# Performance work log

Measured on AMD Instinct MI355X. Metric: run time of the kernel, lower is better.

Reference implementation:

```python
import jax, jax.numpy as jnp
import numpy as np

EPS = 1e-05


def layer_norm(x, a, b):
    m = jnp.mean(x, axis=-1, keepdims=True)
    v = jnp.var(x, axis=-1, keepdims=True)
    return a * (x - m) / jnp.sqrt(v + EPS) + b


def setup_inputs() -> dict:
    key = jax.random.key(0)
    ks = jax.random.split(key, 16)
    b, n, d, h = 1, 384, 128, 128
    s = 1.0 / np.sqrt(d)
    inp = {
        "x": jax.random.normal(ks[0], (b, n, n, d), dtype=jnp.float32),
        "norm_a": jnp.ones((d,), jnp.float32),
        "norm_b": jnp.zeros((d,), jnp.float32),
        "Wl": jax.random.normal(ks[1], (d, h), jnp.float32) * s,
        "bl": jnp.zeros((h,), jnp.float32),
        "Wr": jax.random.normal(ks[2], (d, h), jnp.float32) * s,
        "br": jnp.zeros((h,), jnp.float32),
        "Wlg": jax.random.normal(ks[3], (d, h), jnp.float32) * s,
        "blg": jnp.ones((h,), jnp.float32),
        "Wrg": jax.random.normal(ks[4], (d, h), jnp.float32) * s,
        "brg": jnp.ones((h,), jnp.float32),
        "Wog": jax.random.normal(ks[5], (d, h), jnp.float32) * s,
        "bog": jnp.ones((h,), jnp.float32),
        "on_a": jnp.ones((h,), jnp.float32),
        "on_b": jnp.zeros((h,), jnp.float32),
        "Wo": jax.random.normal(ks[6], (h, d), jnp.float32) * s,
        "bo": jnp.zeros((d,), jnp.float32),
    }
    return inp


def reference(x, norm_a, norm_b, Wl, bl, Wr, br, Wlg, blg, Wrg, brg, Wog, bog, on_a, on_b, Wo, bo):
    n = x.shape[1]
    xn = layer_norm(x, norm_a, norm_b)
    left = (xn @ Wl + bl) * jax.nn.sigmoid(xn @ Wlg + blg)
    right = (xn @ Wr + br) * jax.nn.sigmoid(xn @ Wrg + brg)
    out_gate = jax.nn.sigmoid(xn @ Wog + bog)
    # ingoing mix: out[b,i,j,d] = sum_k left[b,k,j,d] * right[b,k,i,d], in fp32
    out = jnp.einsum('bkjd,bkid->bijd', left.astype(jnp.float32), right.astype(jnp.float32)) / n
    out = out.astype(x.dtype)
    out = layer_norm(out, on_a, on_b) * out_gate
    return out @ Wo + bo
```

## Files before the change

kernel.cpp:

```cpp
#include <hip/hip_runtime.h>
#include <hip/hip_bf16.h>

#define NN 384
#define DD 128
#define MM (NN*NN)
#define IDJ 49152

typedef __attribute__((ext_vector_type(8))) short short8;
typedef __attribute__((ext_vector_type(4))) float f32x4;

__device__ __forceinline__ unsigned short f2bf(float f){
  unsigned u = __float_as_uint(f);
  u += 0x7fffu + ((u >> 16) & 1u);
  return (unsigned short)(u >> 16);
}
__device__ __forceinline__ float bf2f(unsigned short u){
  return __uint_as_float(((unsigned)u) << 16);
}
__device__ __forceinline__ float sigm(float x){
  return 1.0f / (1.0f + __expf(-x));
}
__device__ __forceinline__ unsigned cvtpk(float lo, float hi){
  unsigned r;
  asm("v_cvt_pk_bf16_f32 %0, %1, %2" : "=v"(r) : "v"(lo), "v"(hi));
  return r;
}
__device__ __forceinline__ f32x4 mfma16(short8 a, short8 b, f32x4 c){
  return __builtin_amdgcn_mfma_f32_16x16x32_bf16(a, b, c, 0, 0, 0);
}
__device__ __forceinline__ void gll16(const void* g, void* l){
  __builtin_amdgcn_global_load_lds(
      (const __attribute__((address_space(1))) unsigned int*)g,
      (__attribute__((address_space(3))) unsigned int*)l, 16, 0, 0);
}

__global__ void k_prep(const float* __restrict__ Wl, const float* __restrict__ Wlg,
                       const float* __restrict__ Wr, const float* __restrict__ Wrg,
                       const float* __restrict__ Wog, const float* __restrict__ Wo,
                       unsigned short* __restrict__ Wcat, unsigned short* __restrict__ Wot){
  int n = blockIdx.x;
  if(n < 640){
    const float* src; int col;
    if(n < 128){ src = Wl;  col = n; }
    else if(n < 256){ src = Wlg; col = n-128; }
    else if(n < 384){ src = Wr;  col = n-256; }
    else if(n < 512){ src = Wrg; col = n-384; }
    else            { src = Wog; col = n-512; }
    for(int k = threadIdx.x; k < 128; k += 64)
      Wcat[n*128 + k] = f2bf(src[k*128 + col]);
  } else {
    int c = n - 640;
    for(int k = threadIdx.x; k < 128; k += 64)
      Wot[c*128 + k] = f2bf(Wo[k*128 + c]);
  }
}

__global__ __launch_bounds__(256, 3) void k_lng(
    const float* __restrict__ x, const float* __restrict__ na,
    const float* __restrict__ nb, const unsigned short* __restrict__ Wcat,
    const float* __restrict__ bog,
    unsigned short* __restrict__ xn, unsigned short* __restrict__ gate){
  __shared__ char lds[32768];
  const int tid = threadIdx.x;
  const int wid = tid >> 6, lane = tid & 63;
  const int lrow = lane & 15, lgrp = lane >> 4;
  const long m0 = (long)blockIdx.x * 128;

  float2 a2 = *(const float2*)(na + lane*2);
  float2 b2 = *(const float2*)(nb + lane*2);

  #pragma unroll 2
  for(int b4 = 0; b4 < 8; ++b4){
    float2 v[4];
    #pragma unroll
    for(int s = 0; s < 4; ++s)
      v[s] = *(const float2*)(x + (m0 + wid*32 + b4*4 + s)*DD + lane*2);
    #pragma unroll
    for(int s = 0; s < 4; ++s){
      int r = wid*32 + b4*4 + s;
      float sm = v[s].x + v[s].y, sq = v[s].x*v[s].x + v[s].y*v[s].y;
      #pragma unroll
      for(int m = 32; m >= 1; m >>= 1){ sm += __shfl_xor(sm,m); sq += __shfl_xor(sq,m); }
      float mean = sm*(1.f/128.f);
      float var  = sq*(1.f/128.f) - mean*mean;
      float rstd = rsqrtf(var + 1e-5f);
      unsigned pk = cvtpk(a2.x*(v[s].x-mean)*rstd + b2.x,
                          a2.y*(v[s].y-mean)*rstd + b2.y);
      *(unsigned*)(xn + (m0+r)*DD + lane*2) = pk;
      *(unsigned*)(&lds[r*256 + ((lane*4) ^ ((r&7)<<4))]) = pk;
    }
  }
  __syncthreads();

  f32x4 acc[2][8];
  #pragma unroll
  for(int cf = 0; cf < 2; ++cf){
    int c0 = wid*32 + cf*16 + lgrp*4;
    float4 b4v = *(const float4*)(bog + c0);
    #pragma unroll
    for(int mf = 0; mf < 8; ++mf) acc[cf][mf] = (f32x4){b4v.x,b4v.y,b4v.z,b4v.w};
  }
  #pragma unroll
  for(int ks = 0; ks < 4; ++ks){
    short8 af0 = *(const short8*)(Wcat + (512 + wid*32 + lrow)*DD + ks*32 + lgrp*8);
    short8 af1 = *(const short8*)(Wcat + (512 + wid*32 + 16 + lrow)*DD + ks*32 + lgrp*8);
    #pragma unroll
    for(int mf = 0; mf < 8; ++mf){
      int r = mf*16 + lrow;
      short8 bx = *(const short8*)(&lds[r*256 + (((ks*4+lgrp)*16) ^ ((r&7)<<4))]);
      acc[0][mf] = mfma16(af0, bx, acc[0][mf]);
      acc[1][mf] = mfma16(af1, bx, acc[1][mf]);
    }
  }
  #pragma unroll
  for(int cf = 0; cf < 2; ++cf){
    int c0 = wid*32 + cf*16 + lgrp*4;
    #pragma unroll
    for(int mf = 0; mf < 8; ++mf){
      int rr = mf*16 + lrow;
      uint2 pk;
      pk.x = cvtpk(sigm(acc[cf][mf][0]), sigm(acc[cf][mf][1]));
      pk.y = cvtpk(sigm(acc[cf][mf][2]), sigm(acc[cf][mf][3]));
      *(uint2*)((char*)gate + (m0+rr)*256 + ((c0*2) ^ ((rr&7)<<4))) = pk;
    }
  }
}

__global__ __launch_bounds__(256, 4) void k_proj(
    const unsigned short* __restrict__ xn, const unsigned short* __restrict__ Wcat,
    const float* __restrict__ bl, const float* __restrict__ blg,
    const float* __restrict__ br, const float* __restrict__ brg,
    unsigned short* __restrict__ Lt, unsigned short* __restrict__ Rt){
  __shared__ char lds[2][16384];
  const int tid = threadIdx.x;
  const int wid = tid >> 6, lane = tid & 63;
  const int lrow = lane & 15, lgrp = lane >> 4;
  const int b = blockIdx.x;
  const int f = b / 288;
  const int w = b % 288;

  const int ws = wid >> 1;
  const int wd = wid & 1;
  const int d  = f*32 + wd*16 + lrow;

  short8 bv[4], bg[4];
  #pragma unroll
  for(int ks = 0; ks < 4; ++ks){
    bv[ks] = *(const short8*)(Wcat + (ws*256 + d)*DD + ks*32 + lgrp*8);
    bg[ks] = *(const short8*)(Wcat + (ws*256 + 128 + d)*DD + ks*32 + lgrp*8);
  }
  const float b0v = (ws ? br  : bl )[d];
  const float b1v = (ws ? brg : blg)[d];
  const float sc  = ws ? 1.0f : (1.0f/384.0f);
  unsigned short* const base = (ws ? Rt : Lt) + (long)d*MM;

  auto stage = [&](int buf, int v){
    int j = v/6, kb = v%6;
    int rsub = lane >> 4, c = lane & 15;
    #pragma unroll
    for(int p = 0; p < 4; ++p){
      int r0 = p*16 + wid*4;
      int r = r0 + rsub;
      gll16(xn + ((long)(kb*64 + r)*NN + j)*DD + (c ^ (r & 7))*8, &lds[buf][r0*256]);
    }
  };

  stage(0, w*8);
  __syncthreads();
  int cur = 0;
  for(int i = 0; i < 8; ++i){
    int v = w*8 + i;
    if(i < 7) stage(cur^1, v+1);

    f32x4 zero = {0.f,0.f,0.f,0.f};
    f32x4 acc[4][2];
    #pragma unroll
    for(int a1=0;a1<4;++a1){ acc[a1][0] = zero; acc[a1][1] = zero; }

    #pragma unroll
    for(int ks = 0; ks < 4; ++ks){
      #pragma unroll
      for(int fr = 0; fr < 4; ++fr){
        int r = fr*16 + lrow;
        short8 af = *(const short8*)(&lds[cur][r*256 + (((ks*4+lgrp)*16) ^ ((r&7)<<4))]);
        acc[fr][0] = mfma16(af, bv[ks], acc[fr][0]);
        acc[fr][1] = mfma16(af, bg[ks], acc[fr][1]);
      }
    }

    int j = v/6, kb = v%6;
    unsigned short* dst = base + (long)j*NN + kb*64;
    #pragma unroll
    for(int fr = 0; fr < 4; ++fr){
      float v0 = (acc[fr][0][0] + b0v)*sigm(acc[fr][1][0] + b1v)*sc;
      float v1 = (acc[fr][0][1] + b0v)*sigm(acc[fr][1][1] + b1v)*sc;
      float v2 = (acc[fr][0][2] + b0v)*sigm(acc[fr][1][2] + b1v)*sc;
      float v3 = (acc[fr][0][3] + b0v)*sigm(acc[fr][1][3] + b1v)*sc;
      uint2 pk; pk.x = cvtpk(v0, v1); pk.y = cvtpk(v2, v3);
      *(uint2*)(dst + fr*16 + lgrp*4) = pk;
    }
    __syncthreads();
    cur ^= 1;
  }
}

__global__ __launch_bounds__(256) void k_einsum(
    const unsigned short* __restrict__ Rt, const unsigned short* __restrict__ Lt,
    unsigned short* __restrict__ mid){
  __shared__ char lds[65536];
  const int b = blockIdx.x;
  const int xcd = b & 7, slot = b >> 3;
  const int d = (slot/9)*8 + xcd;
  const int t = slot % 9;
  const int it = t/3, jt = t%3;
  const int i0 = it*128, j0 = jt*128;
  const unsigned short* Abase = Lt + (long)d*MM;
  const unsigned short* Bbase = Rt + (long)d*MM;
  const int wid = threadIdx.x >> 6, lane = threadIdx.x & 63;
  const int wr = wid >> 1, wc = wid & 1;
  const int lrow = lane & 15, lgrp = lane >> 4;

  auto stage = [&](int buf, int kt){
    int k = kt*64;
    int c = lane & 7;
    #pragma unroll
    for(int t8 = 0; t8 < 8; ++t8){
      int rr = wid*64 + t8*8 + (lane >> 3);
      int r = rr & 127;
      const unsigned short* src = (rr < 128) ? (Abase + (long)(j0+r)*NN + k)
                                             : (Bbase + (long)(i0+r)*NN + k);
      gll16(src + (c ^ (r & 7))*8, &lds[buf*32768 + (wid*64 + t8*8)*128]);
    }
  };

  f32x4 zero = {0.f,0.f,0.f,0.f};
  f32x4 acc[4][4];
  #pragma unroll
  for(int a1 = 0; a1 < 4; ++a1)
    #pragma unroll
    for(int a2 = 0; a2 < 4; ++a2) acc[a1][a2] = zero;

  stage(0, 0);
  __syncthreads();
  for(int kt = 0; kt < 6; ++kt){
    int cur = kt & 1;
    if(kt < 5) stage(cur ^ 1, kt + 1);
    const int base = cur*32768;
    #pragma unroll
    for(int ks = 0; ks < 2; ++ks){
      short8 af[4], bf[4];
      #pragma unroll
      for(int f = 0; f < 4; ++f){
        int rj = wr*64 + f*16 + lrow;
        af[f] = *(const short8*)(&lds[base + rj*128 + (((ks*4+lgrp)*16) ^ ((rj & 7) << 4))]);
        int ri = wc*64 + f*16 + lrow;
        bf[f] = *(const short8*)(&lds[base + 16384 + ri*128 + (((ks*4+lgrp)*16) ^ ((ri & 7) << 4))]);
      }
      #pragma unroll
      for(int fj = 0; fj < 4; ++fj)
        #pragma unroll
        for(int fi = 0; fi < 4; ++fi)
          acc[fj][fi] = mfma16(af[fj], bf[fi], acc[fj][fi]);
    }
    __syncthreads();
  }

  #pragma unroll
  for(int fj = 0; fj < 4; ++fj){
    int j = j0 + wr*64 + fj*16 + lgrp*4;
    #pragma unroll
    for(int fi = 0; fi < 4; ++fi){
      int i = i0 + wc*64 + fi*16 + lrow;
      uint2 pk;
      pk.x = cvtpk(acc[fj][fi][0], acc[fj][fi][1]);
      pk.y = cvtpk(acc[fj][fi][2], acc[fj][fi][3]);
      *(uint2*)(mid + (long)i*IDJ + (long)d*NN + j) = pk;
    }
  }
}

__global__ __launch_bounds__(256, 4) void k_final(
    const unsigned short* __restrict__ mid, const unsigned short* __restrict__ gate,
    const float* __restrict__ ona, const float* __restrict__ onb,
    const unsigned short* __restrict__ Wot, const float* __restrict__ bo,
    float* __restrict__ out){
  __shared__ unsigned short midt[64][136];
  __shared__ char gv[16384];
  const int tid = threadIdx.x;
  const int wid = tid >> 6, lane = tid & 63;
  const int lrow = lane & 15, lgrp = lane >> 4;
  const int b = blockIdx.x;
  const int xcd = b & 7, slot = b >> 3;
  const int i = xcd + (slot/6)*8;
  const int j0 = (slot%6)*64;

  {
    const char* gsrc = (const char*)gate + ((long)i*NN + j0)*256;
    #pragma unroll
    for(int p = 0; p < 4; ++p)
      gll16(gsrc + p*4096 + wid*1024 + lane*16, &gv[p*4096 + wid*1024]);
  }
  {
    int jp = tid & 15, dr = tid >> 4;
    const unsigned short* mp = mid + (long)i*IDJ + j0 + jp*4;
    #pragma unroll
    for(int pass = 0; pass < 8; ++pass){
      int dd = pass*16 + dr;
      uint2 v = *(const uint2*)(mp + dd*NN);
      midt[jp*4+0][dd] = (unsigned short)(v.x & 0xffffu);
      midt[jp*4+1][dd] = (unsigned short)(v.x >> 16);
      midt[jp*4+2][dd] = (unsigned short)(v.y & 0xffffu);
      midt[jp*4+3][dd] = (unsigned short)(v.y >> 16);
    }
  }
  __syncthreads();

  {
    int j = tid >> 2, s = tid & 3;
    float vals[32];
    float sum = 0.f, sq = 0.f;
    #pragma unroll
    for(int o8 = 0; o8 < 4; ++o8){
      short8 h = *(const short8*)(&midt[j][s*32 + o8*8]);
      #pragma unroll
      for(int q = 0; q < 8; ++q){
        float vq = bf2f((unsigned short)h[q]);
        vals[o8*8+q] = vq; sum += vq; sq += vq*vq;
      }
    }
    #pragma unroll
    for(int m = 1; m < 4; m <<= 1){ sum += __shfl_xor(sum, m); sq += __shfl_xor(sq, m); }
    float mean = sum*(1.f/128.f);
    float var  = sq *(1.f/128.f) - mean*mean;
    float rstd = rsqrtf(var + 1e-5f);
    #pragma unroll
    for(int o = 0; o < 32; o += 4){
      int dd = s*32 + o;
      char* gp = &gv[j*256 + ((dd*2) ^ ((j&7)<<4))];
      uint2 gvv = *(uint2*)gp;
      float g0 = bf2f((unsigned short)(gvv.x & 0xffffu));
      float g1 = bf2f((unsigned short)(gvv.x >> 16));
      float g2 = bf2f((unsigned short)(gvv.y & 0xffffu));
      float g3 = bf2f((unsigned short)(gvv.y >> 16));
      float4 a4 = *(const float4*)(ona + dd);
      float4 b4 = *(const float4*)(onb + dd);
      float v0 = (a4.x*(vals[o]  -mean)*rstd + b4.x)*g0;
      float v1 = (a4.y*(vals[o+1]-mean)*rstd + b4.y)*g1;
      float v2 = (a4.z*(vals[o+2]-mean)*rstd + b4.z)*g2;
      float v3 = (a4.w*(vals[o+3]-mean)*rstd + b4.w)*g3;
      uint2 pk; pk.x = cvtpk(v0, v1); pk.y = cvtpk(v2, v3);
      *(uint2*)gp = pk;
    }
  }
  __syncthreads();

  {
    f32x4 zero = {0.f,0.f,0.f,0.f};
    f32x4 acc[8];
    #pragma unroll
    for(int fc = 0; fc < 8; ++fc) acc[fc] = zero;
    #pragma unroll 1
    for(int ks = 0; ks < 4; ++ks){
      int row = wid*16 + lrow;
      short8 a = *(const short8*)(&gv[row*256 + (((ks*4+lgrp)*16) ^ ((row & 7) << 4))]);
      #pragma unroll
      for(int fc = 0; fc < 8; ++fc){
        short8 bfr = *(const short8*)(Wot + (fc*16 + lrow)*DD + ks*32 + lgrp*8);
        acc[fc] = mfma16(a, bfr, acc[fc]);
      }
    }
    #pragma unroll
    for(int fc = 0; fc < 8; ++fc){
      int c = fc*16 + lrow;
      float bb = bo[c];
      #pragma unroll
      for(int q = 0; q < 4; ++q){
        int jl = wid*16 + lgrp*4 + q;
        out[((long)i*NN + j0 + jl)*DD + c] = acc[fc][q] + bb;
      }
    }
  }
}

extern "C" void kernel_launch(void* const* d_in, const int* in_sizes, int n_in,
                              void* d_out, int out_size, void* d_ws, size_t ws_size,
                              hipStream_t stream){
  const float* x   = (const float*)d_in[0];
  const float* na  = (const float*)d_in[1];
  const float* nb  = (const float*)d_in[2];
  const float* Wl  = (const float*)d_in[3];
  const float* bl  = (const float*)d_in[4];
  const float* Wr  = (const float*)d_in[5];
  const float* br  = (const float*)d_in[6];
  const float* Wlg = (const float*)d_in[7];
  const float* blg = (const float*)d_in[8];
  const float* Wrg = (const float*)d_in[9];
  const float* brg = (const float*)d_in[10];
  const float* Wog = (const float*)d_in[11];
  const float* bog = (const float*)d_in[12];
  const float* ona = (const float*)d_in[13];
  const float* onb = (const float*)d_in[14];
  const float* Wo  = (const float*)d_in[15];
  const float* bo  = (const float*)d_in[16];
  float* out = (float*)d_out;

  char* ws = (char*)d_ws;
  const size_t SZ = (size_t)MM*DD*2;
  unsigned short* xn   = (unsigned short*)(ws);
  unsigned short* Lt   = (unsigned short*)(ws + SZ);
  unsigned short* Rt   = (unsigned short*)(ws + 2*SZ);
  unsigned short* gate = (unsigned short*)(ws + 3*SZ);
  unsigned short* Wcat = (unsigned short*)(ws + 4*SZ);
  unsigned short* Wot  = (unsigned short*)(ws + 4*SZ + (size_t)640*128*2);
  unsigned short* mid  = xn;

  k_prep  <<<768, 64, 0, stream>>>(Wl, Wlg, Wr, Wrg, Wog, Wo, Wcat, Wot);
  k_lng   <<<1152, 256, 0, stream>>>(x, na, nb, Wcat, bog, xn, gate);
  k_proj  <<<1152, 256, 0, stream>>>(xn, Wcat, bl, blg, br, brg, Lt, Rt);
  k_einsum<<<1152, 256, 0, stream>>>(Rt, Lt, mid);
  k_final <<<2304, 256, 0, stream>>>(mid, gate, ona, onb, Wot, bo, out);
}
```

Before: 203.9 us.

## Block mid tensor in 32-wide j chunks so final kernel loads it with direct LDS copies

The matmul kernel now writes the intermediate in a blocked layout ([i][j/32][d][j%32]), so each 64-row j tile of one i is a contiguous 16KB region. The final kernel fetches that region with global-to-LDS 16-byte loads, the same way as the gate, replacing the strided per-element loads and scalar LDS transpose stores. The layernorm phase then reads scalar bf16 values from LDS at a 64-byte stride, twice per element. This adds LDS read traffic and possible bank conflicts in exchange for cheaper, coalesced global loads.

Result: no change. 204.3 us (+0.2%).

```diff
diff --git a/kernel.cpp b/kernel.cpp
--- a/kernel.cpp
+++ b/kernel.cpp
@@ -274,7 +274,7 @@
       uint2 pk;
       pk.x = cvtpk(acc[fj][fi][0], acc[fj][fi][1]);
       pk.y = cvtpk(acc[fj][fi][2], acc[fj][fi][3]);
-      *(uint2*)(mid + (long)i*IDJ + (long)d*NN + j) = pk;
+      *(uint2*)(mid + (long)i*IDJ + ((j>>5)<<12) + (d<<5) + (j&31)) = pk;
     }
   }
 }
@@ -284,8 +284,8 @@
     const float* __restrict__ ona, const float* __restrict__ onb,
     const unsigned short* __restrict__ Wot, const float* __restrict__ bo,
     float* __restrict__ out){
-  __shared__ unsigned short midt[64][136];
-  __shared__ char gv[16384];
+  __shared__ char M[16384];
+  __shared__ char G[16384];
   const int tid = threadIdx.x;
   const int wid = tid >> 6, lane = tid & 63;
   const int lrow = lane & 15, lgrp = lane >> 4;
@@ -295,48 +295,42 @@
   const int j0 = (slot%6)*64;
 
   {
+    const char* msrc = (const char*)mid + (long)i*98304 + (j0>>5)*8192;
+    #pragma unroll
+    for(int p = 0; p < 4; ++p)
+      gll16(msrc + p*4096 + wid*1024 + lane*16, &M[p*4096 + wid*1024]);
+  }
+  {
     const char* gsrc = (const char*)gate + ((long)i*NN + j0)*256;
     #pragma unroll
     for(int p = 0; p < 4; ++p)
-      gll16(gsrc + p*4096 + wid*1024 + lane*16, &gv[p*4096 + wid*1024]);
-  }
-  {
-    int jp = tid & 15, dr = tid >> 4;
-    const unsigned short* mp = mid + (long)i*IDJ + j0 + jp*4;
-    #pragma unroll
-    for(int pass = 0; pass < 8; ++pass){
-      int dd = pass*16 + dr;
-      uint2 v = *(const uint2*)(mp + dd*NN);
-      midt[jp*4+0][dd] = (unsigned short)(v.x & 0xffffu);
-      midt[jp*4+1][dd] = (unsigned short)(v.x >> 16);
-      midt[jp*4+2][dd] = (unsigned short)(v.y & 0xffffu);
-      midt[jp*4+3][dd] = (unsigned short)(v.y >> 16);
-    }
+      gll16(gsrc + p*4096 + wid*1024 + lane*16, &G[p*4096 + wid*1024]);
   }
   __syncthreads();
 
   {
     int j = tid >> 2, s = tid & 3;
-    float vals[32];
+    const int mrow = (j >> 5)*8192 + (j & 31)*2;
     float sum = 0.f, sq = 0.f;
     #pragma unroll
-    for(int o8 = 0; o8 < 4; ++o8){
-      short8 h = *(const short8*)(&midt[j][s*32 + o8*8]);
-      #pragma unroll
-      for(int q = 0; q < 8; ++q){
-        float vq = bf2f((unsigned short)h[q]);
-        vals[o8*8+q] = vq; sum += vq; sq += vq*vq;
-      }
-    }
-    #pragma unroll
-    for(int m = 1; m < 4; m <<= 1){ sum += __shfl_xor(sum, m); sq += __shfl_xor(sq, m); }
+    for(int o = 0; o < 32; ++o){
+      int d = s*32 + o;
+      float v = bf2f(*(const unsigned short*)(&M[mrow + d*64]));
+      sum += v; sq += v*v;
+    }
+    sum += __shfl_xor(sum, 1); sq += __shfl_xor(sq, 1);
+    sum += __shfl_xor(sum, 2); sq += __shfl_xor(sq, 2);
     float mean = sum*(1.f/128.f);
     float var  = sq *(1.f/128.f) - mean*mean;
     float rstd = rsqrtf(var + 1e-5f);
     #pragma unroll
     for(int o = 0; o < 32; o += 4){
       int dd = s*32 + o;
-      char* gp = &gv[j*256 + ((dd*2) ^ ((j&7)<<4))];
+      float m0 = bf2f(*(const unsigned short*)(&M[mrow + (dd+0)*64]));
+      float m1 = bf2f(*(const unsigned short*)(&M[mrow + (dd+1)*64]));
+      float m2 = bf2f(*(const unsigned short*)(&M[mrow + (dd+2)*64]));
+      float m3 = bf2f(*(const unsigned short*)(&M[mrow + (dd+3)*64]));
+      char* gp = &G[j*256 + ((dd*2) ^ ((j&7)<<4))];
       uint2 gvv = *(uint2*)gp;
       float g0 = bf2f((unsigned short)(gvv.x & 0xffffu));
       float g1 = bf2f((unsigned short)(gvv.x >> 16));
@@ -344,10 +338,10 @@
       float g3 = bf2f((unsigned short)(gvv.y >> 16));
       float4 a4 = *(const float4*)(ona + dd);
       float4 b4 = *(const float4*)(onb + dd);
-      float v0 = (a4.x*(vals[o]  -mean)*rstd + b4.x)*g0;
-      float v1 = (a4.y*(vals[o+1]-mean)*rstd + b4.y)*g1;
-      float v2 = (a4.z*(vals[o+2]-mean)*rstd + b4.z)*g2;
-      float v3 = (a4.w*(vals[o+3]-mean)*rstd + b4.w)*g3;
+      float v0 = (a4.x*(m0-mean)*rstd + b4.x)*g0;
+      float v1 = (a4.y*(m1-mean)*rstd + b4.y)*g1;
+      float v2 = (a4.z*(m2-mean)*rstd + b4.z)*g2;
+      float v3 = (a4.w*(m3-mean)*rstd + b4.w)*g3;
       uint2 pk; pk.x = cvtpk(v0, v1); pk.y = cvtpk(v2, v3);
       *(uint2*)gp = pk;
     }
@@ -362,7 +356,7 @@
     #pragma unroll 1
     for(int ks = 0; ks < 4; ++ks){
       int row = wid*16 + lrow;
-      short8 a = *(const short8*)(&gv[row*256 + (((ks*4+lgrp)*16) ^ ((row & 7) << 4))]);
+      short8 a = *(const short8*)(&G[row*256 + (((ks*4+lgrp)*16) ^ ((row & 7) << 4))]);
       #pragma unroll
       for(int fc = 0; fc < 8; ++fc){
         short8 bfr = *(const short8*)(Wot + (fc*16 + lrow)*DD + ks*32 + lgrp*8);
```
